# Performance work log

Hardware: AMD Instinct MI355X
Metric: run time of the kernel (lower is better)

Reference implementation:

```python
import jax, jax.numpy as jnp
import numpy as np
import math

HID = 256      # hidden_dim
POS = 32       # pos_dim (hardcoded num_pos_feats=32 in pos2embed call)
HEADS = 4
DH = HID // HEADS
B = 8          # number of ragged batches
N = 2048       # points per batch (inputs and queries, equal counts)
LN_EPS = 1e-5


def pos2embed(pos, num_pos_feats=POS):
    # pos: [..., 3] -> [..., 3*num_pos_feats]; faithfully keeps the original
    # bug where pos_z's cos half uses pos_x.
    pos = pos * (2.0 * math.pi)
    dim_t = jnp.arange(num_pos_feats, dtype=jnp.float32)
    dim_t = 2.0 * jnp.floor(dim_t / 2.0) / num_pos_feats + 1.0
    px = pos[..., 0, None] / dim_t
    py = pos[..., 1, None] / dim_t
    pz = pos[..., 2, None] / dim_t
    def interleave(s, c):
        return jnp.stack((s, c), axis=-1).reshape(*s.shape[:-1], -1)
    ex = interleave(jnp.sin(px[..., 0::2]), jnp.cos(px[..., 1::2]))
    ey = interleave(jnp.sin(py[..., 0::2]), jnp.cos(py[..., 1::2]))
    ez = interleave(jnp.sin(pz[..., 0::2]), jnp.cos(px[..., 1::2]))  # original bug
    return jnp.concatenate((ey, ex, ez), axis=-1)


def setup_inputs() -> dict:
    key = jax.random.key(0)
    ks = jax.random.split(key, 16)
    inputs = jax.random.normal(ks[0], (B * N, HID), jnp.float32)
    Q_in = jax.random.normal(ks[1], (B * N, HID), jnp.float32)
    bid = jnp.repeat(jnp.arange(B, dtype=jnp.float32), N)[:, None]
    input_coords = jnp.concatenate([bid, jax.random.uniform(ks[2], (B * N, 3), jnp.float32)], -1)
    Q_in_coords = jnp.concatenate([bid, jax.random.uniform(ks[3], (B * N, 3), jnp.float32)], -1)
    s = 0.02
    Wq = jax.random.normal(ks[4], (HID, HID + POS), jnp.float32) * s
    Wk = jax.random.normal(ks[5], (HID, HID + POS), jnp.float32) * s
    Wv = jax.random.normal(ks[6], (HID, HID + POS), jnp.float32) * s
    in_proj_w = jax.random.normal(ks[7], (3 * HID, HID), jnp.float32) * s
    in_proj_b = jnp.zeros((3 * HID,), jnp.float32)
    out_proj_w = jax.random.normal(ks[8], (HID, HID), jnp.float32) * s
    out_proj_b = jnp.zeros((HID,), jnp.float32)
    ln_g = jnp.ones((HID,), jnp.float32)
    ln_b = jnp.zeros((HID,), jnp.float32)
    pe_w1 = jax.random.normal(ks[9], (POS, POS * 3), jnp.float32) * s
    pe_b1 = jnp.zeros((POS,), jnp.float32)
    pe_w2 = jax.random.normal(ks[10], (POS, POS), jnp.float32) * s
    pe_b2 = jnp.zeros((POS,), jnp.float32)
    return dict(inputs=inputs, Q_in=Q_in, input_coords=input_coords, Q_in_coords=Q_in_coords,
                Wq=Wq, Wk=Wk, Wv=Wv, in_proj_w=in_proj_w, in_proj_b=in_proj_b,
                out_proj_w=out_proj_w, out_proj_b=out_proj_b, ln_g=ln_g, ln_b=ln_b,
                pe_w1=pe_w1, pe_b1=pe_b1, pe_w2=pe_w2, pe_b2=pe_b2)


def reference(inputs, Q_in, input_coords, Q_in_coords, Wq, Wk, Wv,
              in_proj_w, in_proj_b, out_proj_w, out_proj_b, ln_g, ln_b,
              pe_w1, pe_b1, pe_w2, pe_b2):
    # Equal per-batch counts let the ragged per-batch loop be one batched op.
    def pos_mlp(coords):  # [BN,4] -> [B,N,POS]
        e = pos2embed(coords[:, 1:], POS)                   # [BN, 3*POS]
        h = jax.nn.relu(e @ pe_w1.T + pe_b1)
        return (h @ pe_w2.T + pe_b2).reshape(B, N, POS)

    xb = inputs.reshape(B, N, HID)
    qb = Q_in.reshape(B, N, HID)
    ip = jnp.concatenate([xb, pos_mlp(input_coords)], -1)   # [B,N,HID+POS]
    qp = jnp.concatenate([qb, pos_mlp(Q_in_coords)], -1)

    Q = jnp.einsum('bnc,hc->bnh', qp, Wq)
    K = jnp.einsum('bnc,hc->bnh', ip, Wk)
    V = jnp.einsum('bnc,hc->bnh', ip, Wv)

    # nn.MultiheadAttention: its own in_proj on top of Q/K/V, then out_proj
    wq, wk, wv = in_proj_w[:HID], in_proj_w[HID:2 * HID], in_proj_w[2 * HID:]
    bq, bk, bv = in_proj_b[:HID], in_proj_b[HID:2 * HID], in_proj_b[2 * HID:]
    q = (Q @ wq.T + bq).reshape(B, N, HEADS, DH)
    k = (K @ wk.T + bk).reshape(B, N, HEADS, DH)
    v = (V @ wv.T + bv).reshape(B, N, HEADS, DH)

    scores = jnp.einsum('bqhd,bkhd->bhqk', q, k) / math.sqrt(DH)
    attn = jax.nn.softmax(scores, axis=-1)
    o = jnp.einsum('bhqk,bkhd->bqhd', attn, v).reshape(B, N, HID)
    o = o @ out_proj_w.T + out_proj_b

    # residual + LayerNorm (dropout is identity in eval)
    y = qb + o
    mu = y.mean(-1, keepdims=True)
    var = ((y - mu) ** 2).mean(-1, keepdims=True)
    yn = (y - mu) / jnp.sqrt(var + LN_EPS) * ln_g + ln_b
    return yn.reshape(B * N, HID)
```

## Files before the change

kernel.cpp:

```cpp
#include <hip/hip_runtime.h>
#include <math.h>

#define HID 256
#define CIN 288
#define NTOK 16384
#define NSEQ 2048
#define NH 4
#define DHD 64
#define TWO_PI 6.2831853071795864769f

typedef __attribute__((ext_vector_type(8))) short bf16x8;
typedef __attribute__((ext_vector_type(4))) float f32x4;
typedef __attribute__((ext_vector_type(4))) unsigned short u16x4;

__device__ __forceinline__ ushort f2bf(float x) {
    unsigned u = __float_as_uint(x);
    u = (u + 0x7FFFu + ((u >> 16) & 1u)) >> 16;
    return (ushort)u;
}

__device__ __forceinline__ float fast_exp2(float x) {
    return __builtin_amdgcn_exp2f(x);
}

__device__ __forceinline__ unsigned pack_bf_trunc(float a, float b) {
    return __builtin_amdgcn_perm(__float_as_uint(b), __float_as_uint(a), 0x07060302u);
}

__device__ __forceinline__ void gload_lds16(const ushort* g, ushort* l) {
    __builtin_amdgcn_global_load_lds(
        (const __attribute__((address_space(1))) unsigned*)g,
        (__attribute__((address_space(3))) unsigned*)l, 16, 0, 0);
}

__device__ __forceinline__ int sw(int row) {
    return (((row >> 3) << 1) ^ row) & 7;
}

__device__ __forceinline__ int swv(int row) {
    return ((row & 3) ^ ((row >> 2) & 3));
}

__global__ __launch_bounds__(256) void prep_kernel(
        const float* __restrict__ icoords, const float* __restrict__ qcoords,
        const float* __restrict__ w1, const float* __restrict__ b1,
        const float* __restrict__ w2, const float* __restrict__ b2,
        const float* __restrict__ X, const float* __restrict__ Qin,
        const float* __restrict__ inW,
        const float* __restrict__ Wq, const float* __restrict__ Wk,
        const float* __restrict__ Wv,
        const float* __restrict__ Wo,
        ushort* __restrict__ ip, ushort* __restrict__ qp,
        ushort* __restrict__ Wb, ushort* __restrict__ WoB) {
    __shared__ float SMEM[4160];
    const int blk = blockIdx.x;
    const int t = threadIdx.x;

    if (blk < 1024) {
        float* sw1t = SMEM;
        float* sb1  = SMEM + 3072;
        float* sw2  = SMEM + 3104;
        float* sb2  = SMEM + 4128;
        for (int i = t; i < 96 * 32; i += 256) {
            const int e = i >> 5, r = i & 31;
            sw1t[i] = w1[r * 96 + e];
        }
        for (int i = t; i < 32 * 32; i += 256) sw2[i] = w2[i];
        if (t < 32) { sb1[t] = b1[t]; sb2[t] = b2[t]; }
        __syncthreads();

        const int p = t & 7;
        const int tok = blk * 32 + (t >> 3);
        const int which = tok >> 14;
        const int m = tok & (NTOK - 1);
        const float* cr = (which ? qcoords : icoords) + m * 4;
        const float x = cr[1] * TWO_PI;
        const float y = cr[2] * TWO_PI;
        const float z = cr[3] * TWO_PI;

        f32x4 h = *(const f32x4*)&sb1[4 * p];

        for (int jj = 0; jj < 16; ++jj) {
            const float inv = 1.0f / (1.0f + 0.0625f * (float)jj);
            const float xs = x * inv, ys = y * inv, zs = z * inv;
            const float cx = __cosf(xs);
            float vals[6];
            int idx[6];
            vals[0] = __sinf(ys);  idx[0] = 2 * jj;
            vals[1] = __cosf(ys);  idx[1] = 2 * jj + 1;
            vals[2] = __sinf(xs);  idx[2] = 32 + 2 * jj;
            vals[3] = cx;          idx[3] = 32 + 2 * jj + 1;
            vals[4] = __sinf(zs);  idx[4] = 64 + 2 * jj;
            vals[5] = cx;          idx[5] = 64 + 2 * jj + 1;
#pragma unroll
            for (int u = 0; u < 6; ++u)
                h += vals[u] * *(const f32x4*)&sw1t[idx[u] * 32 + 4 * p];
        }
#pragma unroll
        for (int j = 0; j < 4; ++j) h[j] = fmaxf(h[j], 0.f);

        float part[32];
#pragma unroll
        for (int c = 0; c < 32; ++c) {
            const f32x4 w4 = *(const f32x4*)&sw2[c * 32 + 4 * p];
            part[c] = (h[0] * w4[0] + h[1] * w4[1]) + (h[2] * w4[2] + h[3] * w4[3]);
        }
#pragma unroll
        for (int c = 0; c < 32; ++c) part[c] += __shfl_xor(part[c], 1);
#pragma unroll
        for (int c = 0; c < 32; ++c) part[c] += __shfl_xor(part[c], 2);
#pragma unroll
        for (int c = 0; c < 32; ++c) part[c] += __shfl_xor(part[c], 4);

        ushort* dst = (which ? qp : ip) + (size_t)m * CIN + 256;
        u16x4 w;
#pragma unroll
        for (int r = 0; r < 4; ++r) w[r] = f2bf(sb2[4 * p + r] + part[4 * p + r]);
        *(u16x4*)(dst + 4 * p) = w;
    } else if (blk < 1088) {
        const int f = ((blk - 1024) * 256 + t) * 4;
        const float4 a = *(const float4*)(Wo + f);
        u16x4 o = {f2bf(a.x), f2bf(a.y), f2bf(a.z), f2bf(a.w)};
        *(u16x4*)(WoB + f) = o;
    } else if (blk < 1856) {
        float* wrow = SMEM;
        const int idx = blk - 1088;
        const int o = idx & 255;
        const int mat = idx >> 8;
        wrow[t] = inW[(mat * 256 + o) * 256 + t];
        __syncthreads();
        const float* Wm = (mat == 0) ? Wq : ((mat == 1) ? Wk : Wv);
        const int t2 = 256 + (t & 31);
        float acc0 = 0.f, acc1 = 0.f;
#pragma unroll 4
        for (int h = 0; h < 256; ++h) {
            const float wh = wrow[h];
            acc0 += wh * Wm[h * CIN + t];
            acc1 += wh * Wm[h * CIN + t2];
        }
        ushort* dst = Wb + (size_t)(mat * 256 + o) * CIN;
        dst[t] = f2bf(acc0);
        if (t < 32) dst[t2] = f2bf(acc1);
    } else {
        const int i = blk - 1856;
        const int which = i >> 11;
        const size_t f = ((size_t)(i & 2047) * 256 + t) * 8;
        const int row = (int)(f >> 8);
        const int col = (int)(f & 255);
        const float* src = which ? Qin : X;
        ushort* dst = which ? qp : ip;
        const float4 a = *(const float4*)(src + f);
        const float4 b = *(const float4*)(src + f + 4);
        u16x4 o0 = {f2bf(a.x), f2bf(a.y), f2bf(a.z), f2bf(a.w)};
        u16x4 o1 = {f2bf(b.x), f2bf(b.y), f2bf(b.z), f2bf(b.w)};
        *(u16x4*)(dst + (size_t)row * CIN + col) = o0;
        *(u16x4*)(dst + (size_t)row * CIN + col + 4) = o1;
    }
}

__global__ __launch_bounds__(256) void qkv_mfma(
        const ushort* __restrict__ qp, const ushort* __restrict__ ip,
        const ushort* __restrict__ Wb, const float* __restrict__ bias,
        ushort* __restrict__ qout, ushort* __restrict__ kout, ushort* __restrict__ vout) {
    __shared__ ushort SA[2 * 4096];
    const int wv = threadIdx.x >> 6, lane = threadIdx.x & 63;
    const int l16 = lane & 15, quad = lane >> 4;
    const int m0b = blockIdx.x * 128;
    const int y = blockIdx.y;
    const int mat = y >> 2;
    const int n0 = y * 64;
    const ushort* A = (mat == 0) ? qp : ip;

    size_t asrc[2];
    int adst[2];
#pragma unroll
    for (int i = 0; i < 2; ++i) {
        const int idx = wv * 128 + i * 64 + lane;
        const int row = idx >> 2, cc = idx & 3;
        asrc[i] = (size_t)(m0b + row) * CIN + cc * 8;
        adst[i] = (wv * 128 + i * 64) * 8;
    }
    int aoff[2];
#pragma unroll
    for (int s = 0; s < 2; ++s)
        aoff[s] = ((32 * wv + 16 * s + l16) * 4 + quad) * 8;

    f32x4 acc[2][4];
#pragma unroll
    for (int s = 0; s < 2; ++s)
#pragma unroll
        for (int c = 0; c < 4; ++c) acc[s][c] = (f32x4){0.f, 0.f, 0.f, 0.f};

#pragma unroll
    for (int i = 0; i < 2; ++i)
        gload_lds16(A + asrc[i], SA + adst[i]);

    for (int t = 0; t < 9; ++t) {
        __syncthreads();
        if (t + 1 < 9) {
            const int bo = ((t + 1) & 1) * 4096;
#pragma unroll
            for (int i = 0; i < 2; ++i)
                gload_lds16(A + asrc[i] + (t + 1) * 32, SA + bo + adst[i]);
        }
        const ushort* buf = SA + (t & 1) * 4096;
        const int kk = t * 32;
        bf16x8 af[2], bf[4];
#pragma unroll
        for (int s = 0; s < 2; ++s)
            af[s] = *(const bf16x8*)(buf + aoff[s]);
#pragma unroll
        for (int c = 0; c < 4; ++c)
            bf[c] = *(const bf16x8*)(Wb + (size_t)(n0 + 16 * c + l16) * CIN + kk + quad * 8);
        if (mat < 2) {
#pragma unroll
            for (int s = 0; s < 2; ++s)
#pragma unroll
                for (int c = 0; c < 4; ++c)
                    acc[s][c] = __builtin_amdgcn_mfma_f32_16x16x32_bf16(bf[c], af[s], acc[s][c], 0, 0, 0);
        } else {
#pragma unroll
            for (int s = 0; s < 2; ++s)
#pragma unroll
                for (int c = 0; c < 4; ++c)
                    acc[s][c] = __builtin_amdgcn_mfma_f32_16x16x32_bf16(af[s], bf[c], acc[s][c], 0, 0, 0);
        }
    }

    const int h = y & 3;
    const int m0 = m0b + wv * 32;
    if (mat < 2) {
        const float scale = (mat == 0) ? (0.125f * 1.44269504088896f) : 1.0f;
        ushort* out = (mat == 0) ? qout : kout;
#pragma unroll
        for (int s = 0; s < 2; ++s) {
            const int tokm = m0 + 16 * s + l16;
            const int b = tokm >> 11, nn = tokm & (NSEQ - 1);
#pragma unroll
            for (int c = 0; c < 4; ++c) {
                const f32x4 b4 = *(const f32x4*)&bias[n0 + 16 * c + quad * 4];
                u16x4 w;
#pragma unroll
                for (int r = 0; r < 4; ++r) w[r] = f2bf((acc[s][c][r] + b4[r]) * scale);
                *(u16x4*)(out + ((size_t)(b * NH + h) * NSEQ + nn) * DHD + 16 * c + quad * 4) = w;
            }
        }
    } else {
#pragma unroll
        for (int s = 0; s < 2; ++s) {
            const int tok0 = m0 + 16 * s + quad * 4;
            const int b = tok0 >> 11, nn0 = tok0 & (NSEQ - 1);
#pragma unroll
            for (int c = 0; c < 4; ++c) {
                const int d = 16 * c + l16;
                const float bv = bias[n0 + d];
                u16x4 w;
#pragma unroll
                for (int r = 0; r < 4; ++r) w[r] = f2bf(acc[s][c][r] + bv);
                *(u16x4*)(vout + ((size_t)(b * NH + h) * DHD + d) * NSEQ + nn0) = w;
            }
        }
    }
}

__global__ __launch_bounds__(512, 4) void attn_kernel(
        const ushort* __restrict__ q, const ushort* __restrict__ k,
        const ushort* __restrict__ v, ushort* __restrict__ out) {
    __shared__ ushort SL[24576];
    const int bh = blockIdx.y;
    const int wv = threadIdx.x >> 6;
    const int grp = wv >> 2;
    const int wq = wv & 3;
    const int lane = threadIdx.x & 63;
    const int l16 = lane & 15, quad = lane >> 4;
    const int q0 = blockIdx.x * 128 + wq * 32;

    const ushort* qb = q + (size_t)bh * NSEQ * DHD;
    const ushort* kb = k + (size_t)bh * NSEQ * DHD + (size_t)(grp * 1024) * DHD;
    const ushort* vb = v + (size_t)bh * DHD * NSEQ + grp * 1024;
    ushort* SG = SL + grp * 12288;

    bf16x8 qf[2][2];
#pragma unroll
    for (int s = 0; s < 2; ++s)
#pragma unroll
        for (int hh = 0; hh < 2; ++hh)
            qf[s][hh] = *(const bf16x8*)(qb + (size_t)(q0 + 16 * s + l16) * DHD + 32 * hh + quad * 8);

    const int krow_s = 8 * wq + (lane >> 3);
    const int kcg = (lane & 7) ^ sw(krow_s);
    const size_t ksrc = (size_t)krow_s * DHD + kcg * 8;
    const int kdst = wq * 512;
    const int vrow_s = 16 * wq + (lane >> 2);
    const int vcg = (lane & 3) ^ swv(vrow_s);
    const size_t vsrc = (size_t)vrow_s * NSEQ + vcg * 8;
    const int vdst = wq * 512;

    const int krow = 8 * (l16 >> 2) + (l16 & 3);
    int koff[2][2];
    int voff[4];
#pragma unroll
    for (int m = 0; m < 2; ++m) {
        const int row = krow + 4 * m;
#pragma unroll
        for (int hh = 0; hh < 2; ++hh)
            koff[m][hh] = row * 64 + (((hh * 4 + quad) ^ sw(row))) * 8;
    }
#pragma unroll
    for (int c = 0; c < 4; ++c) {
        const int d = 16 * c + l16;
        voff[c] = 2048 + d * 32 + ((quad ^ swv(d))) * 8;
    }

    f32x4 Oc[2][4];
#pragma unroll
    for (int s = 0; s < 2; ++s)
#pragma unroll
        for (int c = 0; c < 4; ++c) Oc[s][c] = (f32x4){0.f, 0.f, 0.f, 0.f};
    float lr[2] = {0.f, 0.f};

#pragma unroll
    for (int pt = 0; pt < 2; ++pt) {
        ushort* db = SG + pt * 4096;
        gload_lds16(kb + (size_t)(pt * 32) * DHD + ksrc, db + kdst);
        gload_lds16(vb + pt * 32 + vsrc, db + 2048 + vdst);
    }

    int co = 0, po = 8192;
    for (int t = 0; t < 32; ++t) {
        if (t < 31) asm volatile("s_waitcnt vmcnt(2)" ::: "memory");
        else        asm volatile("s_waitcnt vmcnt(0)" ::: "memory");
        __builtin_amdgcn_s_barrier();

        if (t < 30) {
            ushort* db = SG + po;
            gload_lds16(kb + (size_t)((t + 2) * 32) * DHD + ksrc, db + kdst);
            gload_lds16(vb + (t + 2) * 32 + vsrc, db + 2048 + vdst);
            po = (po == 8192) ? 0 : po + 4096;
        }
        const ushort* buf = SG + co;
        co = (co == 8192) ? 0 : co + 4096;

        bf16x8 kf[2][2], vf[4];
#pragma unroll
        for (int m = 0; m < 2; ++m)
#pragma unroll
            for (int hh = 0; hh < 2; ++hh)
                kf[m][hh] = *(const bf16x8*)(buf + koff[m][hh]);
#pragma unroll
        for (int c = 0; c < 4; ++c)
            vf[c] = *(const bf16x8*)(buf + voff[c]);

#pragma unroll
        for (int s = 0; s < 2; ++s) {
            f32x4 s0 = (f32x4){0.f, 0.f, 0.f, 0.f};
            f32x4 s1 = (f32x4){0.f, 0.f, 0.f, 0.f};
            s0 = __builtin_amdgcn_mfma_f32_16x16x32_bf16(kf[0][0], qf[s][0], s0, 0, 0, 0);
            s0 = __builtin_amdgcn_mfma_f32_16x16x32_bf16(kf[0][1], qf[s][1], s0, 0, 0, 0);
            s1 = __builtin_amdgcn_mfma_f32_16x16x32_bf16(kf[1][0], qf[s][0], s1, 0, 0, 0);
            s1 = __builtin_amdgcn_mfma_f32_16x16x32_bf16(kf[1][1], qf[s][1], s1, 0, 0, 0);

            float p0[4], p1[4];
#pragma unroll
            for (int r = 0; r < 4; ++r) {
                p0[r] = fast_exp2(s0[r]);
                p1[r] = fast_exp2(s1[r]);
            }
            lr[s] += (p0[0] + p0[1]) + (p0[2] + p0[3]) + (p1[0] + p1[1]) + (p1[2] + p1[3]);

            union { bf16x8 v8; unsigned d[4]; } P;
            P.d[0] = pack_bf_trunc(p0[0], p0[1]);
            P.d[1] = pack_bf_trunc(p0[2], p0[3]);
            P.d[2] = pack_bf_trunc(p1[0], p1[1]);
            P.d[3] = pack_bf_trunc(p1[2], p1[3]);
#pragma unroll
            for (int c = 0; c < 4; ++c)
                Oc[s][c] = __builtin_amdgcn_mfma_f32_16x16x32_bf16(vf[c], P.v8, Oc[s][c], 0, 0, 0);
        }
    }

#pragma unroll
    for (int s = 0; s < 2; ++s) {
        lr[s] += __shfl_xor(lr[s], 16);
        lr[s] += __shfl_xor(lr[s], 32);
    }

    __syncthreads();
    float* exch = (float*)SL;
    float* lx   = ((float*)SL) + 128 * 68;
    if (grp == 1) {
#pragma unroll
        for (int s = 0; s < 2; ++s) {
            const int lq = wq * 32 + 16 * s + l16;
#pragma unroll
            for (int c = 0; c < 4; ++c)
                *(f32x4*)&exch[lq * 68 + 16 * c + 4 * quad] = Oc[s][c];
            if (quad == 0) lx[lq] = lr[s];
        }
    }
    __syncthreads();
    if (grp == 0) {
        const int b = bh >> 2, h = bh & 3;
#pragma unroll
        for (int s = 0; s < 2; ++s) {
            const int lq = wq * 32 + 16 * s + l16;
            const float linv = 1.0f / (lr[s] + lx[lq]);
            ushort* dst = out + (size_t)(b * NSEQ + blockIdx.x * 128 + lq) * HID + h * DHD;
#pragma unroll
            for (int c = 0; c < 4; ++c) {
                const f32x4 o1 = *(const f32x4*)&exch[lq * 68 + 16 * c + 4 * quad];
                u16x4 w;
#pragma unroll
                for (int r = 0; r < 4; ++r) w[r] = f2bf((Oc[s][c][r] + o1[r]) * linv);
                *(u16x4*)(dst + 16 * c + quad * 4) = w;
            }
        }
    }
}

__global__ __launch_bounds__(256) void oproj_ln_mfma(
        const ushort* __restrict__ abuf, const float* __restrict__ Qin,
        const ushort* __restrict__ WoB, const float* __restrict__ bo,
        const float* __restrict__ g, const float* __restrict__ be,
        float* __restrict__ out) {
    __shared__ float yt[32][260];
    const int wv = threadIdx.x >> 6, lane = threadIdx.x & 63;
    const int l16 = lane & 15, quad = lane >> 4;
    const int m0 = blockIdx.x * 32;
    const int n0 = wv * 64;

    f32x4 acc[2][4];
#pragma unroll
    for (int s = 0; s < 2; ++s)
#pragma unroll
        for (int c = 0; c < 4; ++c) acc[s][c] = (f32x4){0.f, 0.f, 0.f, 0.f};

    for (int kk = 0; kk < HID; kk += 32) {
        bf16x8 af[2], bf[4];
#pragma unroll
        for (int s = 0; s < 2; ++s)
            af[s] = *(const bf16x8*)(abuf + (size_t)(m0 + 16 * s + l16) * HID + kk + quad * 8);
#pragma unroll
        for (int c = 0; c < 4; ++c)
            bf[c] = *(const bf16x8*)(WoB + (size_t)(n0 + 16 * c + l16) * HID + kk + quad * 8);
#pragma unroll
        for (int s = 0; s < 2; ++s)
#pragma unroll
            for (int c = 0; c < 4; ++c)
                acc[s][c] = __builtin_amdgcn_mfma_f32_16x16x32_bf16(af[s], bf[c], acc[s][c], 0, 0, 0);
    }

#pragma unroll
    for (int s = 0; s < 2; ++s)
#pragma unroll
        for (int c = 0; c < 4; ++c) {
            const int col = n0 + 16 * c + l16;
            const float bv = bo[col];
#pragma unroll
            for (int r = 0; r < 4; ++r) {
                const int row = 16 * s + quad * 4 + r;
                yt[row][col] = acc[s][c][r] + bv + Qin[(size_t)(m0 + row) * HID + col];
            }
        }
    __syncthreads();

    float gv[4], bev[4];
#pragma unroll
    for (int u = 0; u < 4; ++u) { gv[u] = g[lane + 64 * u]; bev[u] = be[lane + 64 * u]; }

    for (int rr = 0; rr < 8; ++rr) {
        const int row = wv * 8 + rr;
        float sm = 0.f, ssq = 0.f;
        float yv[4];
#pragma unroll
        for (int u = 0; u < 4; ++u) {
            yv[u] = yt[row][lane + 64 * u];
            sm += yv[u]; ssq += yv[u] * yv[u];
        }
#pragma unroll
        for (int off = 32; off >= 1; off >>= 1) {
            sm += __shfl_xor(sm, off);
            ssq += __shfl_xor(ssq, off);
        }
        const float mu = sm * (1.f / 256.f);
        const float rs = rsqrtf(fmaxf(ssq * (1.f / 256.f) - mu * mu, 0.f) + 1e-5f);
        float* dst = out + (size_t)(m0 + row) * HID;
#pragma unroll
        for (int u = 0; u < 4; ++u)
            dst[lane + 64 * u] = (yv[u] - mu) * rs * gv[u] + bev[u];
    }
}

extern "C" void kernel_launch(void* const* d_in, const int* in_sizes, int n_in,
                              void* d_out, int out_size, void* d_ws, size_t ws_size,
                              hipStream_t stream) {
    const float* inputs       = (const float*)d_in[0];
    const float* Q_in         = (const float*)d_in[1];
    const float* input_coords = (const float*)d_in[2];
    const float* Q_in_coords  = (const float*)d_in[3];
    const float* Wq           = (const float*)d_in[4];
    const float* Wk           = (const float*)d_in[5];
    const float* Wv           = (const float*)d_in[6];
    const float* in_proj_w    = (const float*)d_in[7];
    const float* in_proj_b    = (const float*)d_in[8];
    const float* out_proj_w   = (const float*)d_in[9];
    const float* out_proj_b   = (const float*)d_in[10];
    const float* ln_g         = (const float*)d_in[11];
    const float* ln_b         = (const float*)d_in[12];
    const float* pe_w1        = (const float*)d_in[13];
    const float* pe_b1        = (const float*)d_in[14];
    const float* pe_w2        = (const float*)d_in[15];
    const float* pe_b2        = (const float*)d_in[16];

    char* ws = (char*)d_ws;
    ushort* Wb   = (ushort*)(ws);
    ushort* WoB  = (ushort*)(ws + 442368);
    ushort* qp   = (ushort*)(ws + 573440);
    ushort* ip   = (ushort*)(ws + 10010624);
    ushort* qbuf = (ushort*)(ws + 19447808);
    ushort* kbuf = (ushort*)(ws + 27836416);
    ushort* vbuf = (ushort*)(ws + 36225024);
    ushort* abuf = (ushort*)(ws + 44613632);

    prep_kernel<<<5952, 256, 0, stream>>>(input_coords, Q_in_coords,
                                          pe_w1, pe_b1, pe_w2, pe_b2,
                                          inputs, Q_in, in_proj_w,
                                          Wq, Wk, Wv, out_proj_w,
                                          ip, qp, Wb, WoB);
    qkv_mfma<<<dim3(128, 12), 256, 0, stream>>>(qp, ip, Wb, in_proj_b,
                                                qbuf, kbuf, vbuf);
    attn_kernel<<<dim3(16, 32), 512, 0, stream>>>(qbuf, kbuf, vbuf, abuf);
    oproj_ln_mfma<<<512, 256, 0, stream>>>(abuf, Q_in, WoB, out_proj_b,
                                           ln_g, ln_b, (float*)d_out);
}
```

Before: 223.7 us.

## Triple-buffer QKV GEMM with swizzled LDS weights and halve oproj tile rows

The QKV GEMM moves from a double-buffered A-only LDS pipeline to a three-stage pipeline that also stages the weight tile in LDS, using an XOR swizzle to avoid bank conflicts. It waits with explicit vmcnt counts instead of a full syncthreads, so loads two steps ahead overlap with MFMA work. Separately, the output-projection+LayerNorm kernel uses 16-row tiles and twice as many blocks to improve occupancy, at the cost of reloading the weights more often. The extra LDS use could reduce occupancy in the QKV kernel.

```diff
diff --git a/kernel.cpp b/kernel.cpp
--- a/kernel.cpp
+++ b/kernel.cpp
@@ -162,7 +162,7 @@
         const ushort* __restrict__ qp, const ushort* __restrict__ ip,
         const ushort* __restrict__ Wb, const float* __restrict__ bias,
         ushort* __restrict__ qout, ushort* __restrict__ kout, ushort* __restrict__ vout) {
-    __shared__ ushort SA[2 * 4096];
+    __shared__ ushort SA[3 * 6144];
     const int wv = threadIdx.x >> 6, lane = threadIdx.x & 63;
     const int l16 = lane & 15, quad = lane >> 4;
     const int m0b = blockIdx.x * 128;
@@ -176,14 +176,26 @@
 #pragma unroll
     for (int i = 0; i < 2; ++i) {
         const int idx = wv * 128 + i * 64 + lane;
-        const int row = idx >> 2, cc = idx & 3;
+        const int row = idx >> 2;
+        const int cc = (idx & 3) ^ ((row >> 1) & 3);
         asrc[i] = (size_t)(m0b + row) * CIN + cc * 8;
         adst[i] = (wv * 128 + i * 64) * 8;
     }
+    const int bidx = wv * 64 + lane;
+    const int brow = bidx >> 2;
+    const int bcc = (bidx & 3) ^ ((brow >> 1) & 3);
+    const size_t bsrc = (size_t)(n0 + brow) * CIN + bcc * 8;
+    const int bdst = 4096 + wv * 512;
+
+    const int rsw = quad ^ ((l16 >> 1) & 3);
     int aoff[2];
 #pragma unroll
     for (int s = 0; s < 2; ++s)
-        aoff[s] = ((32 * wv + 16 * s + l16) * 4 + quad) * 8;
+        aoff[s] = ((32 * wv + 16 * s + l16) * 4 + rsw) * 8;
+    int boff[4];
+#pragma unroll
+    for (int c = 0; c < 4; ++c)
+        boff[c] = 4096 + ((16 * c + l16) * 4 + rsw) * 8;
 
     f32x4 acc[2][4];
 #pragma unroll
@@ -192,26 +204,36 @@
         for (int c = 0; c < 4; ++c) acc[s][c] = (f32x4){0.f, 0.f, 0.f, 0.f};
 
 #pragma unroll
-    for (int i = 0; i < 2; ++i)
-        gload_lds16(A + asrc[i], SA + adst[i]);
-
+    for (int pt = 0; pt < 2; ++pt) {
+        ushort* db = SA + pt * 6144;
+        gload_lds16(A + asrc[0] + pt * 32, db + adst[0]);
+        gload_lds16(A + asrc[1] + pt * 32, db + adst[1]);
+        gload_lds16(Wb + bsrc + pt * 32, db + bdst);
+    }
+
+    int co = 0, po = 12288;
     for (int t = 0; t < 9; ++t) {
-        __syncthreads();
-        if (t + 1 < 9) {
-            const int bo = ((t + 1) & 1) * 4096;
-#pragma unroll
-            for (int i = 0; i < 2; ++i)
-                gload_lds16(A + asrc[i] + (t + 1) * 32, SA + bo + adst[i]);
-        }
-        const ushort* buf = SA + (t & 1) * 4096;
-        const int kk = t * 32;
+        if (t < 8) asm volatile("s_waitcnt vmcnt(3)" ::: "memory");
+        else       asm volatile("s_waitcnt vmcnt(0)" ::: "memory");
+        __builtin_amdgcn_s_barrier();
+
+        if (t + 2 < 9) {
+            ushort* db = SA + po;
+            gload_lds16(A + asrc[0] + (t + 2) * 32, db + adst[0]);
+            gload_lds16(A + asrc[1] + (t + 2) * 32, db + adst[1]);
+            gload_lds16(Wb + bsrc + (t + 2) * 32, db + bdst);
+            po = (po == 12288) ? 0 : po + 6144;
+        }
+        const ushort* buf = SA + co;
+        co = (co == 12288) ? 0 : co + 6144;
+
         bf16x8 af[2], bf[4];
 #pragma unroll
         for (int s = 0; s < 2; ++s)
             af[s] = *(const bf16x8*)(buf + aoff[s]);
 #pragma unroll
         for (int c = 0; c < 4; ++c)
-            bf[c] = *(const bf16x8*)(Wb + (size_t)(n0 + 16 * c + l16) * CIN + kk + quad * 8);
+            bf[c] = *(const bf16x8*)(buf + boff[c]);
         if (mat < 2) {
 #pragma unroll
             for (int s = 0; s < 2; ++s)
@@ -423,53 +445,45 @@
         const ushort* __restrict__ WoB, const float* __restrict__ bo,
         const float* __restrict__ g, const float* __restrict__ be,
         float* __restrict__ out) {
-    __shared__ float yt[32][260];
+    __shared__ float yt[16][260];
     const int wv = threadIdx.x >> 6, lane = threadIdx.x & 63;
     const int l16 = lane & 15, quad = lane >> 4;
-    const int m0 = blockIdx.x * 32;
+    const int m0 = blockIdx.x * 16;
     const int n0 = wv * 64;
 
-    f32x4 acc[2][4];
-#pragma unroll
-    for (int s = 0; s < 2; ++s)
-#pragma unroll
-        for (int c = 0; c < 4; ++c) acc[s][c] = (f32x4){0.f, 0.f, 0.f, 0.f};
+    f32x4 acc[4];
+#pragma unroll
+    for (int c = 0; c < 4; ++c) acc[c] = (f32x4){0.f, 0.f, 0.f, 0.f};
 
     for (int kk = 0; kk < HID; kk += 32) {
-        bf16x8 af[2], bf[4];
-#pragma unroll
-        for (int s = 0; s < 2; ++s)
-            af[s] = *(const bf16x8*)(abuf + (size_t)(m0 + 16 * s + l16) * HID + kk + quad * 8);
+        const bf16x8 af = *(const bf16x8*)(abuf + (size_t)(m0 + l16) * HID + kk + quad * 8);
+        bf16x8 bf[4];
 #pragma unroll
         for (int c = 0; c < 4; ++c)
             bf[c] = *(const bf16x8*)(WoB + (size_t)(n0 + 16 * c + l16) * HID + kk + quad * 8);
 #pragma unroll
-        for (int s = 0; s < 2; ++s)
-#pragma unroll
-            for (int c = 0; c < 4; ++c)
-                acc[s][c] = __builtin_amdgcn_mfma_f32_16x16x32_bf16(af[s], bf[c], acc[s][c], 0, 0, 0);
-    }
-
-#pragma unroll
-    for (int s = 0; s < 2; ++s)
-#pragma unroll
-        for (int c = 0; c < 4; ++c) {
-            const int col = n0 + 16 * c + l16;
-            const float bv = bo[col];
-#pragma unroll
-            for (int r = 0; r < 4; ++r) {
-                const int row = 16 * s + quad * 4 + r;
-                yt[row][col] = acc[s][c][r] + bv + Qin[(size_t)(m0 + row) * HID + col];
-            }
-        }
+        for (int c = 0; c < 4; ++c)
+            acc[c] = __builtin_amdgcn_mfma_f32_16x16x32_bf16(af, bf[c], acc[c], 0, 0, 0);
+    }
+
+#pragma unroll
+    for (int c = 0; c < 4; ++c) {
+        const int col = n0 + 16 * c + l16;
+        const float bv = bo[col];
+#pragma unroll
+        for (int r = 0; r < 4; ++r) {
+            const int row = quad * 4 + r;
+            yt[row][col] = acc[c][r] + bv + Qin[(size_t)(m0 + row) * HID + col];
+        }
+    }
     __syncthreads();
 
     float gv[4], bev[4];
 #pragma unroll
     for (int u = 0; u < 4; ++u) { gv[u] = g[lane + 64 * u]; bev[u] = be[lane + 64 * u]; }
 
-    for (int rr = 0; rr < 8; ++rr) {
-        const int row = wv * 8 + rr;
+    for (int rr = 0; rr < 4; ++rr) {
+        const int row = wv * 4 + rr;
         float sm = 0.f, ssq = 0.f;
         float yv[4];
 #pragma unroll
@@ -530,6 +544,6 @@
     qkv_mfma<<<dim3(128, 12), 256, 0, stream>>>(qp, ip, Wb, in_proj_b,
                                                 qbuf, kbuf, vbuf);
     attn_kernel<<<dim3(16, 32), 512, 0, stream>>>(qbuf, kbuf, vbuf, abuf);
-    oproj_ln_mfma<<<512, 256, 0, stream>>>(abuf, Q_in, WoB, out_proj_b,
-                                           ln_g, ln_b, (float*)d_out);
-}
+    oproj_ln_mfma<<<1024, 256, 0, stream>>>(abuf, Q_in, WoB, out_proj_b,
+                                            ln_g, ln_b, (float*)d_out);
+}
```

Measured after the change: 225.0 us. No clear change (+0.6%).
